# Optimization experiments

Measured on AMD Instinct MI355X. Metric: run time of the kernel, lower is better.

## Reference

```python
import jax, jax.numpy as jnp
import numpy as np

B, S, H, E, TOPK = 16384, 64, 256, 8, 2


def setup_inputs() -> dict:
    key = jax.random.key(0)
    k1, k2, k3, k4 = jax.random.split(key, 4)
    x = jax.random.normal(k1, (B, S, H), dtype=jnp.float32)
    xr = jax.random.normal(k2, (B, H), dtype=jnp.float32)
    W_router = jax.random.normal(k3, (H, E), dtype=jnp.float32) * 0.02
    W_experts = jax.random.normal(k4, (E, H, H), dtype=jnp.float32) * 0.02
    b_experts = jnp.zeros((E, H), dtype=jnp.float32)
    return {"x": x, "xr": xr, "W_router": W_router,
            "W_experts": W_experts, "b_experts": b_experts}


def reference(x, xr, W_router, W_experts, b_experts):
    # Routing network: logits [B, E]
    logits = xr @ W_router
    # top-2 expert selection; softmax over the two selected logits (as in torch code)
    top_vals, top_idx = jax.lax.top_k(logits, TOPK)          # [B, 2]
    w = jax.nn.softmax(top_vals, axis=1)                     # [B, 2]
    # Dense gate matrix [B, E]: scatter top-2 weights into expert slots
    gate = jnp.zeros_like(logits).at[jnp.arange(x.shape[0])[:, None], top_idx].add(w)
    # Expert forward: pooled token representation -> per-expert dense tanh
    pooled = x.mean(axis=1)                                  # [B, H]
    h_all = jnp.tanh(jnp.einsum('bh,ehd->bed', pooled, W_experts) + b_experts[None])
    # Weighted scatter-add combine: prediction[b] += w * hidden_states
    prediction = jnp.einsum('be,beh->bh', gate, h_all)       # [B, H]
    return prediction
```

## Files before the change

kernel.cpp:

```cpp
#include <hip/hip_runtime.h>
#include <hip/hip_bf16.h>

constexpr int Bn = 16384;
constexpr int S  = 64;
constexpr int H  = 256;
constexpr int E  = 8;

constexpr int RPB   = 32;
constexpr int CBLK  = Bn / RPB;
constexpr int PSTR  = H + 8;
constexpr int POOLB = Bn / 4;
constexpr int PREPB = E * 8;

typedef short bf16x8 __attribute__((ext_vector_type(8)));
typedef float f32x4  __attribute__((ext_vector_type(4)));

__device__ __forceinline__ float fast_tanh(float x) {
    const float ex = __expf(2.0f * x);
    return (ex - 1.0f) / (ex + 1.0f);
}

__global__ __launch_bounds__(256) void stage1_kernel(
    const float* __restrict__ x,
    const float* __restrict__ We,
    __hip_bfloat16* __restrict__ pws,
    __hip_bfloat16* __restrict__ Wf)
{
    __shared__ __hip_bfloat16 tile[32][H + 4];
    const int t = threadIdx.x;

    if (blockIdx.x < POOLB) {
        const int row = blockIdx.x * 4 + (t >> 6);
        const int c4  = t & 63;

        const f32x4* xrow = reinterpret_cast<const f32x4*>(x + (size_t)row * (S * H));
        f32x4 a0 = 0.f, a1 = 0.f, a2 = 0.f, a3 = 0.f;
#pragma unroll 16
        for (int s = 0; s < S; s += 4) {
            f32x4 v0 = xrow[(s + 0) * 64 + c4];
            f32x4 v1 = xrow[(s + 1) * 64 + c4];
            f32x4 v2 = xrow[(s + 2) * 64 + c4];
            f32x4 v3 = xrow[(s + 3) * 64 + c4];
            a0 += v0; a1 += v1; a2 += v2; a3 += v3;
        }
        const f32x4 res = (a0 + a1) + (a2 + a3);
        const float sc = 1.0f / (float)S;
        ushort4 pk;
        {
            __hip_bfloat16 h0 = __float2bfloat16(res[0] * sc);
            __hip_bfloat16 h1 = __float2bfloat16(res[1] * sc);
            __hip_bfloat16 h2 = __float2bfloat16(res[2] * sc);
            __hip_bfloat16 h3 = __float2bfloat16(res[3] * sc);
            pk.x = *reinterpret_cast<unsigned short*>(&h0);
            pk.y = *reinterpret_cast<unsigned short*>(&h1);
            pk.z = *reinterpret_cast<unsigned short*>(&h2);
            pk.w = *reinterpret_cast<unsigned short*>(&h3);
        }
        *reinterpret_cast<ushort4*>(pws + (size_t)row * H + c4 * 4) = pk;
    } else {
        const int bid = blockIdx.x - POOLB;
        const int e   = bid >> 3;
        const int kk  = bid & 7;

        const float* src = We + ((size_t)e * H + kk * 32) * H;
#pragma unroll
        for (int i = 0; i < 8; ++i) {
            const int idx = t + 256 * i;
            const int hh  = idx >> 6;
            const int c4  = idx & 63;
            float4 v = reinterpret_cast<const float4*>(src + (size_t)hh * H)[c4];
            tile[hh][c4 * 4 + 0] = __float2bfloat16(v.x);
            tile[hh][c4 * 4 + 1] = __float2bfloat16(v.y);
            tile[hh][c4 * 4 + 2] = __float2bfloat16(v.z);
            tile[hh][c4 * 4 + 3] = __float2bfloat16(v.w);
        }
        __syncthreads();

#pragma unroll
        for (int i = 0; i < 4; ++i) {
            const int task = i * 256 + t;
            const int nt_  = task >> 6;
            const int l    = task & 63;
            const int hlb  = (l >> 4) * 8;
            const int d    = nt_ * 16 + (l & 15);
            bf16x8 p;
#pragma unroll
            for (int j = 0; j < 8; ++j) {
                __hip_bfloat16 hv = tile[hlb + j][d];
                p[j] = *reinterpret_cast<short*>(&hv);
            }
            reinterpret_cast<bf16x8*>(Wf)[(((size_t)(e * 8 + kk) * 16 + nt_) * 64 + l)] = p;
        }
    }
}

__global__ __launch_bounds__(512, 2) void combine_kernel(
    const __hip_bfloat16* __restrict__ pws,
    const float* __restrict__ xr,
    const float* __restrict__ Wr,
    const float* __restrict__ be,
    const __hip_bfloat16* __restrict__ Wf,
    float* __restrict__ out)
{
    const int b0 = blockIdx.x * RPB;
    const int t  = threadIdx.x;

    __shared__ __hip_bfloat16 pooled[RPB][PSTR];
    __shared__ float logit_s[RPB][E];
    __shared__ float gate_s[RPB][E];

    {
        const __hip_bfloat16* src = pws + (size_t)b0 * H + t * 16;
#pragma unroll
        for (int u = 0; u < 2; ++u) {
            const int g = t * 16 + u * 8;
            bf16x8 v = *reinterpret_cast<const bf16x8*>(src + u * 8);
            *reinterpret_cast<bf16x8*>(&pooled[g >> 8][g & 255]) = v;
        }
    }

    if (t < RPB * E) {
        const int r = t >> 3, e = t & 7;
        const float* xrp = xr + (size_t)(b0 + r) * H;
        double acc = 0.0;
#pragma unroll 8
        for (int h = 0; h < H; ++h)
            acc += (double)xrp[h] * (double)Wr[h * E + e];
        logit_s[r][e] = (float)acc;
    }
    __syncthreads();

    if (t < RPB) {
        int i0 = 0; float v0 = logit_s[t][0];
#pragma unroll
        for (int e = 1; e < E; ++e)
            if (logit_s[t][e] > v0) { v0 = logit_s[t][e]; i0 = e; }
        int i1 = -1; float v1 = -3.0e38f;
#pragma unroll
        for (int e = 0; e < E; ++e) {
            if (e == i0) continue;
            if (logit_s[t][e] > v1) { v1 = logit_s[t][e]; i1 = e; }
        }
        const float ex  = expf(v1 - v0);
        const float inv = 1.0f / (1.0f + ex);
#pragma unroll
        for (int e = 0; e < E; ++e) gate_s[t][e] = 0.f;
        gate_s[t][i0] = inv;
        gate_s[t][i1] = ex * inv;
    }
    __syncthreads();

    {
        const int w  = t >> 6;
        const int l  = t & 63;
        const int mg = w >> 2;
        const int dg = w & 3;
        const int lr = l & 15;
        const int lq = l >> 4;

        f32x4 oacc[4];
#pragma unroll
        for (int n = 0; n < 4; ++n) oacc[n] = 0.f;

        const __hip_bfloat16* abase = &pooled[mg * 16 + lr][lq * 8];
        const bf16x8* wf8 = reinterpret_cast<const bf16x8*>(Wf);

        for (int e = 0; e < E; ++e) {
            f32x4 acc[4];
#pragma unroll
            for (int n = 0; n < 4; ++n) acc[n] = 0.f;

#pragma unroll
            for (int kk = 0; kk < 8; ++kk) {
                const bf16x8 a = *reinterpret_cast<const bf16x8*>(abase + kk * 32);
                const size_t kb = ((size_t)(e * 8 + kk) * 16 + dg * 4) * 64 + l;
                bf16x8 bfr[4];
#pragma unroll
                for (int n = 0; n < 4; ++n)
                    bfr[n] = wf8[kb + (size_t)n * 64];
#pragma unroll
                for (int n = 0; n < 4; ++n)
                    acc[n] = __builtin_amdgcn_mfma_f32_16x16x32_bf16(a, bfr[n], acc[n], 0, 0, 0);
            }

            float g[4];
#pragma unroll
            for (int j = 0; j < 4; ++j) g[j] = gate_s[mg * 16 + lq * 4 + j][e];
#pragma unroll
            for (int n = 0; n < 4; ++n) {
                const int d = dg * 64 + n * 16 + lr;
                const float bias = be[e * H + d];
#pragma unroll
                for (int j = 0; j < 4; ++j)
                    oacc[n][j] += g[j] * fast_tanh(acc[n][j] + bias);
            }
        }

#pragma unroll
        for (int n = 0; n < 4; ++n) {
            const int d = dg * 64 + n * 16 + lr;
#pragma unroll
            for (int j = 0; j < 4; ++j) {
                const int r = mg * 16 + lq * 4 + j;
                out[(size_t)(b0 + r) * H + d] = oacc[n][j];
            }
        }
    }
}

__global__ __launch_bounds__(256) void moe_fused_fallback(
    const float* __restrict__ x, const float* __restrict__ xr,
    const float* __restrict__ Wr, const float* __restrict__ We,
    const float* __restrict__ be, float* __restrict__ out)
{
    const int b = blockIdx.x;
    const int t = threadIdx.x;

    __shared__ float  pooled[H];
    __shared__ float  xr_s[H];
    __shared__ float4 red4[4][64];
    __shared__ float  logits_s[E];
    __shared__ int    sel[2];
    __shared__ float  wsel[2];

    {
        const float4* xrow = reinterpret_cast<const float4*>(x + (size_t)b * S * H);
        const int c4 = t & 63;
        const int sg = t >> 6;
        float4 acc = make_float4(0.f, 0.f, 0.f, 0.f);
#pragma unroll
        for (int i = 0; i < 16; ++i) {
            float4 v = xrow[(sg + 4 * i) * 64 + c4];
            acc.x += v.x; acc.y += v.y; acc.z += v.z; acc.w += v.w;
        }
        red4[sg][c4] = acc;
        xr_s[t] = xr[(size_t)b * H + t];
    }
    __syncthreads();
    {
        const float* r0 = reinterpret_cast<const float*>(&red4[0][0]);
        const float* r1 = reinterpret_cast<const float*>(&red4[1][0]);
        const float* r2 = reinterpret_cast<const float*>(&red4[2][0]);
        const float* r3 = reinterpret_cast<const float*>(&red4[3][0]);
        pooled[t] = (r0[t] + r1[t] + r2[t] + r3[t]) * (1.0f / (float)S);
    }
    if (t < E) {
        double acc = 0.0;
        for (int h = 0; h < H; ++h)
            acc += (double)xr_s[h] * (double)Wr[h * E + t];
        logits_s[t] = (float)acc;
    }
    __syncthreads();
    if (t == 0) {
        int i0 = 0; float v0 = logits_s[0];
        for (int e = 1; e < E; ++e)
            if (logits_s[e] > v0) { v0 = logits_s[e]; i0 = e; }
        int i1 = -1; float v1 = -3.0e38f;
        for (int e = 0; e < E; ++e) {
            if (e == i0) continue;
            if (logits_s[e] > v1) { v1 = logits_s[e]; i1 = e; }
        }
        const float ex = expf(v1 - v0);
        const float inv = 1.0f / (1.0f + ex);
        sel[0] = i0; sel[1] = i1;
        wsel[0] = inv; wsel[1] = ex * inv;
    }
    __syncthreads();
    {
        const int   e0 = sel[0], e1 = sel[1];
        const float w0 = wsel[0], w1 = wsel[1];
        const float* W0 = We + (size_t)e0 * H * H + t;
        const float* W1 = We + (size_t)e1 * H * H + t;
        float a0 = be[e0 * H + t];
        float a1 = be[e1 * H + t];
#pragma unroll 8
        for (int h = 0; h < H; ++h) {
            const float p = pooled[h];
            a0 = fmaf(p, W0[(size_t)h * H], a0);
            a1 = fmaf(p, W1[(size_t)h * H], a1);
        }
        out[(size_t)b * H + t] = w0 * tanhf(a0) + w1 * tanhf(a1);
    }
}

extern "C" void kernel_launch(void* const* d_in, const int* in_sizes, int n_in,
                              void* d_out, int out_size, void* d_ws, size_t ws_size,
                              hipStream_t stream) {
    const float* x  = (const float*)d_in[0];
    const float* xr = (const float*)d_in[1];
    const float* Wr = (const float*)d_in[2];
    const float* We = (const float*)d_in[3];
    const float* be = (const float*)d_in[4];
    float* out = (float*)d_out;

    (void)in_sizes; (void)n_in; (void)out_size;

    const size_t wf_elems = (size_t)E * H * H;
    const size_t need = (wf_elems + (size_t)Bn * H) * sizeof(__hip_bfloat16);
    if (ws_size >= need) {
        __hip_bfloat16* Wf  = (__hip_bfloat16*)d_ws;
        __hip_bfloat16* pws = Wf + wf_elems;
        stage1_kernel<<<POOLB + PREPB, 256, 0, stream>>>(x, We, pws, Wf);
        combine_kernel<<<CBLK, 512, 0, stream>>>(pws, xr, Wr, be, Wf, out);
    } else {
        moe_fused_fallback<<<Bn, 256, 0, stream>>>(x, xr, Wr, We, be, out);
    }
}
```

Before: 256.7 us.

## Fuse sequence mean-pooling into the MFMA combine kernel and shrink row tile

Removes the bf16 pooled-activation workspace by computing the mean over S directly inside the combine kernel, with nontemporal loads of x into shared memory. Weight conversion becomes a separate small prep kernel launched first. Rows per block drop from 32 to 16 and blocks from 512 to 256 threads, one wave per 64-column output slice. This avoids the pooled write and read-back and lets streaming of x overlap with MFMA work from other blocks. The cost is that every block rereads the full 1 MB bf16 expert weights for only 16 rows, doubling weight traffic through cache. Pooling inside each block is also serialized before its matmul phase.

```diff
diff --git a/kernel.cpp b/kernel.cpp
--- a/kernel.cpp
+++ b/kernel.cpp
@@ -6,10 +6,9 @@
 constexpr int H  = 256;
 constexpr int E  = 8;
 
-constexpr int RPB   = 32;
-constexpr int CBLK  = Bn / RPB;
+constexpr int RPB   = 16;
+constexpr int FBLK  = Bn / RPB;
 constexpr int PSTR  = H + 8;
-constexpr int POOLB = Bn / 4;
 constexpr int PREPB = E * 8;
 
 typedef short bf16x8 __attribute__((ext_vector_type(8)));
@@ -20,82 +19,47 @@
     return (ex - 1.0f) / (ex + 1.0f);
 }
 
-__global__ __launch_bounds__(256) void stage1_kernel(
+__global__ __launch_bounds__(256) void prep_kernel(const float* __restrict__ We,
+                                                   __hip_bfloat16* __restrict__ Wf) {
+    __shared__ __hip_bfloat16 tile[32][H + 4];
+    const int bid = blockIdx.x;
+    const int t   = threadIdx.x;
+    const int e   = bid >> 3;
+    const int kk  = bid & 7;
+
+    const float* src = We + ((size_t)e * H + kk * 32) * H;
+#pragma unroll
+    for (int i = 0; i < 8; ++i) {
+        const int idx = t + 256 * i;
+        const int hh  = idx >> 6;
+        const int c4  = idx & 63;
+        float4 v = reinterpret_cast<const float4*>(src + (size_t)hh * H)[c4];
+        tile[hh][c4 * 4 + 0] = __float2bfloat16(v.x);
+        tile[hh][c4 * 4 + 1] = __float2bfloat16(v.y);
+        tile[hh][c4 * 4 + 2] = __float2bfloat16(v.z);
+        tile[hh][c4 * 4 + 3] = __float2bfloat16(v.w);
+    }
+    __syncthreads();
+
+#pragma unroll
+    for (int i = 0; i < 4; ++i) {
+        const int task = i * 256 + t;
+        const int nt_  = task >> 6;
+        const int l    = task & 63;
+        const int hlb  = (l >> 4) * 8;
+        const int d    = nt_ * 16 + (l & 15);
+        bf16x8 p;
+#pragma unroll
+        for (int j = 0; j < 8; ++j) {
+            __hip_bfloat16 hv = tile[hlb + j][d];
+            p[j] = *reinterpret_cast<short*>(&hv);
+        }
+        reinterpret_cast<bf16x8*>(Wf)[(((size_t)(e * 8 + kk) * 16 + nt_) * 64 + l)] = p;
+    }
+}
+
+__global__ __launch_bounds__(256) void fused_kernel(
     const float* __restrict__ x,
-    const float* __restrict__ We,
-    __hip_bfloat16* __restrict__ pws,
-    __hip_bfloat16* __restrict__ Wf)
-{
-    __shared__ __hip_bfloat16 tile[32][H + 4];
-    const int t = threadIdx.x;
-
-    if (blockIdx.x < POOLB) {
-        const int row = blockIdx.x * 4 + (t >> 6);
-        const int c4  = t & 63;
-
-        const f32x4* xrow = reinterpret_cast<const f32x4*>(x + (size_t)row * (S * H));
-        f32x4 a0 = 0.f, a1 = 0.f, a2 = 0.f, a3 = 0.f;
-#pragma unroll 16
-        for (int s = 0; s < S; s += 4) {
-            f32x4 v0 = xrow[(s + 0) * 64 + c4];
-            f32x4 v1 = xrow[(s + 1) * 64 + c4];
-            f32x4 v2 = xrow[(s + 2) * 64 + c4];
-            f32x4 v3 = xrow[(s + 3) * 64 + c4];
-            a0 += v0; a1 += v1; a2 += v2; a3 += v3;
-        }
-        const f32x4 res = (a0 + a1) + (a2 + a3);
-        const float sc = 1.0f / (float)S;
-        ushort4 pk;
-        {
-            __hip_bfloat16 h0 = __float2bfloat16(res[0] * sc);
-            __hip_bfloat16 h1 = __float2bfloat16(res[1] * sc);
-            __hip_bfloat16 h2 = __float2bfloat16(res[2] * sc);
-            __hip_bfloat16 h3 = __float2bfloat16(res[3] * sc);
-            pk.x = *reinterpret_cast<unsigned short*>(&h0);
-            pk.y = *reinterpret_cast<unsigned short*>(&h1);
-            pk.z = *reinterpret_cast<unsigned short*>(&h2);
-            pk.w = *reinterpret_cast<unsigned short*>(&h3);
-        }
-        *reinterpret_cast<ushort4*>(pws + (size_t)row * H + c4 * 4) = pk;
-    } else {
-        const int bid = blockIdx.x - POOLB;
-        const int e   = bid >> 3;
-        const int kk  = bid & 7;
-
-        const float* src = We + ((size_t)e * H + kk * 32) * H;
-#pragma unroll
-        for (int i = 0; i < 8; ++i) {
-            const int idx = t + 256 * i;
-            const int hh  = idx >> 6;
-            const int c4  = idx & 63;
-            float4 v = reinterpret_cast<const float4*>(src + (size_t)hh * H)[c4];
-            tile[hh][c4 * 4 + 0] = __float2bfloat16(v.x);
-            tile[hh][c4 * 4 + 1] = __float2bfloat16(v.y);
-            tile[hh][c4 * 4 + 2] = __float2bfloat16(v.z);
-            tile[hh][c4 * 4 + 3] = __float2bfloat16(v.w);
-        }
-        __syncthreads();
-
-#pragma unroll
-        for (int i = 0; i < 4; ++i) {
-            const int task = i * 256 + t;
-            const int nt_  = task >> 6;
-            const int l    = task & 63;
-            const int hlb  = (l >> 4) * 8;
-            const int d    = nt_ * 16 + (l & 15);
-            bf16x8 p;
-#pragma unroll
-            for (int j = 0; j < 8; ++j) {
-                __hip_bfloat16 hv = tile[hlb + j][d];
-                p[j] = *reinterpret_cast<short*>(&hv);
-            }
-            reinterpret_cast<bf16x8*>(Wf)[(((size_t)(e * 8 + kk) * 16 + nt_) * 64 + l)] = p;
-        }
-    }
-}
-
-__global__ __launch_bounds__(512, 2) void combine_kernel(
-    const __hip_bfloat16* __restrict__ pws,
     const float* __restrict__ xr,
     const float* __restrict__ Wr,
     const float* __restrict__ be,
@@ -110,12 +74,34 @@
     __shared__ float gate_s[RPB][E];
 
     {
-        const __hip_bfloat16* src = pws + (size_t)b0 * H + t * 16;
-#pragma unroll
-        for (int u = 0; u < 2; ++u) {
-            const int g = t * 16 + u * 8;
-            bf16x8 v = *reinterpret_cast<const bf16x8*>(src + u * 8);
-            *reinterpret_cast<bf16x8*>(&pooled[g >> 8][g & 255]) = v;
+        const int w  = t >> 6;
+        const int c4 = t & 63;
+        for (int rr = 0; rr < 4; ++rr) {
+            const int r   = w * 4 + rr;
+            const f32x4* xrow = reinterpret_cast<const f32x4*>(x + (size_t)(b0 + r) * (S * H));
+            f32x4 a0 = 0.f, a1 = 0.f, a2 = 0.f, a3 = 0.f;
+#pragma unroll 16
+            for (int s = 0; s < S; s += 4) {
+                f32x4 v0 = __builtin_nontemporal_load(xrow + (s + 0) * 64 + c4);
+                f32x4 v1 = __builtin_nontemporal_load(xrow + (s + 1) * 64 + c4);
+                f32x4 v2 = __builtin_nontemporal_load(xrow + (s + 2) * 64 + c4);
+                f32x4 v3 = __builtin_nontemporal_load(xrow + (s + 3) * 64 + c4);
+                a0 += v0; a1 += v1; a2 += v2; a3 += v3;
+            }
+            const f32x4 res = (a0 + a1) + (a2 + a3);
+            const float sc = 1.0f / (float)S;
+            ushort4 pk;
+            {
+                __hip_bfloat16 h0 = __float2bfloat16(res[0] * sc);
+                __hip_bfloat16 h1 = __float2bfloat16(res[1] * sc);
+                __hip_bfloat16 h2 = __float2bfloat16(res[2] * sc);
+                __hip_bfloat16 h3 = __float2bfloat16(res[3] * sc);
+                pk.x = *reinterpret_cast<unsigned short*>(&h0);
+                pk.y = *reinterpret_cast<unsigned short*>(&h1);
+                pk.z = *reinterpret_cast<unsigned short*>(&h2);
+                pk.w = *reinterpret_cast<unsigned short*>(&h3);
+            }
+            *reinterpret_cast<ushort4*>(&pooled[r][c4 * 4]) = pk;
         }
     }
 
@@ -151,10 +137,8 @@
     __syncthreads();
 
     {
-        const int w  = t >> 6;
+        const int dg = t >> 6;
         const int l  = t & 63;
-        const int mg = w >> 2;
-        const int dg = w & 3;
         const int lr = l & 15;
         const int lq = l >> 4;
 
@@ -162,7 +146,7 @@
 #pragma unroll
         for (int n = 0; n < 4; ++n) oacc[n] = 0.f;
 
-        const __hip_bfloat16* abase = &pooled[mg * 16 + lr][lq * 8];
+        const __hip_bfloat16* abase = &pooled[lr][lq * 8];
         const bf16x8* wf8 = reinterpret_cast<const bf16x8*>(Wf);
 
         for (int e = 0; e < E; ++e) {
@@ -185,7 +169,7 @@
 
             float g[4];
 #pragma unroll
-            for (int j = 0; j < 4; ++j) g[j] = gate_s[mg * 16 + lq * 4 + j][e];
+            for (int j = 0; j < 4; ++j) g[j] = gate_s[lq * 4 + j][e];
 #pragma unroll
             for (int n = 0; n < 4; ++n) {
                 const int d = dg * 64 + n * 16 + lr;
@@ -201,7 +185,7 @@
             const int d = dg * 64 + n * 16 + lr;
 #pragma unroll
             for (int j = 0; j < 4; ++j) {
-                const int r = mg * 16 + lq * 4 + j;
+                const int r = lq * 4 + j;
                 out[(size_t)(b0 + r) * H + d] = oacc[n][j];
             }
         }
@@ -295,13 +279,11 @@
 
     (void)in_sizes; (void)n_in; (void)out_size;
 
-    const size_t wf_elems = (size_t)E * H * H;
-    const size_t need = (wf_elems + (size_t)Bn * H) * sizeof(__hip_bfloat16);
-    if (ws_size >= need) {
-        __hip_bfloat16* Wf  = (__hip_bfloat16*)d_ws;
-        __hip_bfloat16* pws = Wf + wf_elems;
-        stage1_kernel<<<POOLB + PREPB, 256, 0, stream>>>(x, We, pws, Wf);
-        combine_kernel<<<CBLK, 512, 0, stream>>>(pws, xr, Wr, be, Wf, out);
+    const size_t wf_bytes = (size_t)E * H * H * sizeof(__hip_bfloat16);
+    if (ws_size >= wf_bytes) {
+        __hip_bfloat16* Wf = (__hip_bfloat16*)d_ws;
+        prep_kernel<<<PREPB, 256, 0, stream>>>(We, Wf);
+        fused_kernel<<<FBLK, 256, 0, stream>>>(x, xr, Wr, be, Wf, out);
     } else {
         moe_fused_fallback<<<Bn, 256, 0, stream>>>(x, xr, Wr, We, be, out);
     }
```

New measurement: 268.4 us. 1.05x slower.
